# Kernel tuning notes

Measured on AMD Instinct MI355X. Metric: run time of the kernel, lower is better.

The kernel has to match this reference:

```python
import jax, jax.numpy as jnp
import numpy as np

N, E, B, DIM, NF, EF, HID = 16384, 32768, 512, 64, 14, 4, 128

def _p(key, shape, scale):
    return jax.random.normal(key, shape, dtype=jnp.float32) * scale

def setup_inputs() -> dict:
    key = jax.random.key(0)
    ks = jax.random.split(key, 20)
    s = lambda fan: 1.0 / float(np.sqrt(fan))
    z = lambda *sh: jnp.zeros(sh, jnp.float32)
    return {
        "x": jax.random.normal(ks[0], (N, NF), dtype=jnp.float32),
        "edge_index": jax.random.randint(ks[1], (2, E), 0, N),
        "edge_attr": jax.random.uniform(ks[2], (E, EF), dtype=jnp.float32),
        "batch": jnp.sort(jax.random.randint(ks[3], (N,), 0, B)),
        "do_dropout": 0,
        "mlp_drop": 0,
        "lin0_w": _p(ks[4], (NF, DIM), s(NF)), "lin0_b": z(DIM),
        "nn1_w": _p(ks[5], (EF, HID), s(EF)), "nn1_b": z(HID),
        "nn2_w": _p(ks[6], (HID, DIM * DIM), s(HID)), "nn2_b": z(DIM * DIM),
        "root_w": _p(ks[7], (DIM, DIM), s(DIM)), "conv_b": z(DIM),
        "gru_w_ih": _p(ks[8], (3 * DIM, DIM), s(DIM)), "gru_w_hh": _p(ks[9], (3 * DIM, DIM), s(DIM)),
        "gru_b_ih": _p(ks[10], (3 * DIM,), s(DIM)), "gru_b_hh": _p(ks[11], (3 * DIM,), s(DIM)),
        "lstm_w_ih": _p(ks[12], (4 * DIM, 2 * DIM), s(DIM)), "lstm_w_hh": _p(ks[13], (4 * DIM, DIM), s(DIM)),
        "lstm_b_ih": _p(ks[14], (4 * DIM,), s(DIM)), "lstm_b_hh": _p(ks[15], (4 * DIM,), s(DIM)),
        "lin1_w": _p(ks[16], (2 * DIM, DIM), s(2 * DIM)), "lin1_b": z(DIM),
        "lin2_w": _p(ks[17], (DIM, 1), s(DIM)), "lin2_b": z(1),
    }

def _forward(x, edge_attr, lin0_w, lin0_b, nn1_w, nn1_b, nn2_w, nn2_b, root_w, conv_b,
             gru_w_ih, gru_w_hh, gru_b_ih, gru_b_hh,
             lstm_w_ih, lstm_w_hh, lstm_b_ih, lstm_b_hh,
             lin1_w, lin1_b, lin2_w, lin2_b, edge_index, batch):
    src, dst = edge_index[0], edge_index[1]
    out = jax.nn.relu(x @ lin0_w + lin0_b)                      # [N, DIM]
    h = out
    # Edge-conditioned weights (edge_attr is layer-independent -> compute once)
    ew = jax.nn.relu(edge_attr @ nn1_w + nn1_b) @ nn2_w + nn2_b  # [E, DIM*DIM]
    ew = ew.reshape(E, DIM, DIM)
    deg = jax.ops.segment_sum(jnp.ones((E,), jnp.float32), dst, num_segments=N)
    deg = jnp.maximum(deg, 1.0)[:, None]                        # mean aggregation denominator

    def gru_cell(xin, hprev):
        gi = xin @ gru_w_ih.T + gru_b_ih
        gh = hprev @ gru_w_hh.T + gru_b_hh
        ir, iz, inn = jnp.split(gi, 3, axis=-1)
        hr, hz, hn = jnp.split(gh, 3, axis=-1)
        r = jax.nn.sigmoid(ir + hr)
        zg = jax.nn.sigmoid(iz + hz)
        n = jnp.tanh(inn + r * hn)
        return (1.0 - zg) * n + zg * hprev

    for _ in range(3):  # 3 message-passing rounds (structurally fixed)
        msg = jnp.einsum('ed,edf->ef', out[src], ew)            # gather -> per-edge matvec
        agg = jax.ops.segment_sum(msg, dst, num_segments=N) / deg
        m = jax.nn.relu(out @ root_w + agg + conv_b)            # NNConv (root weight + mean aggr)
        h = gru_cell(m, h)
        out = h

    # Set2Set pooling, 3 processing steps
    q_star = jnp.zeros((B, 2 * DIM), jnp.float32)
    hl = jnp.zeros((B, DIM), jnp.float32)
    cl = jnp.zeros((B, DIM), jnp.float32)
    for _ in range(3):
        gates = q_star @ lstm_w_ih.T + lstm_b_ih + hl @ lstm_w_hh.T + lstm_b_hh
        ii, ff, gg, oo = jnp.split(gates, 4, axis=-1)
        cl = jax.nn.sigmoid(ff) * cl + jax.nn.sigmoid(ii) * jnp.tanh(gg)
        hl = jax.nn.sigmoid(oo) * jnp.tanh(cl)
        q = hl                                                  # [B, DIM]
        e = jnp.sum(out * q[batch], axis=-1)                    # [N]
        emax = jax.ops.segment_max(e, batch, num_segments=B)
        ex = jnp.exp(e - emax[batch])
        esum = jnp.maximum(jax.ops.segment_sum(ex, batch, num_segments=B), 1e-16)
        a = ex / esum[batch]                                    # segment softmax
        r = jax.ops.segment_sum(a[:, None] * out, batch, num_segments=B)
        q_star = jnp.concatenate([q, r], axis=-1)               # [B, 2*DIM]

    y = jax.nn.relu(q_star @ lin1_w + lin1_b)
    # dropout flags are False (eval) -> identity
    y = y @ lin2_w + lin2_b
    return y.reshape(-1)                                        # [B]

def reference(x, edge_index, edge_attr, batch, do_dropout, mlp_drop,
              lin0_w, lin0_b, nn1_w, nn1_b, nn2_w, nn2_b, root_w, conv_b,
              gru_w_ih, gru_w_hh, gru_b_ih, gru_b_hh,
              lstm_w_ih, lstm_w_hh, lstm_b_ih, lstm_b_hh,
              lin1_w, lin1_b, lin2_w, lin2_b):
    return _forward(x, edge_attr, lin0_w, lin0_b, nn1_w, nn1_b, nn2_w, nn2_b, root_w, conv_b,
                    gru_w_ih, gru_w_hh, gru_b_ih, gru_b_hh,
                    lstm_w_ih, lstm_w_hh, lstm_b_ih, lstm_b_hh,
                    lin1_w, lin1_b, lin2_w, lin2_b, edge_index, batch)
```

## Files before the change

kernel.cpp:

```cpp
#include <hip/hip_runtime.h>
#include <math.h>

#define N_NODES 16384
#define N_EDGES 32768
#define NGRAPH  512
#define DIM     64
#define NF      14
#define HIDN    128
#define EWCOLS  4096

typedef unsigned short u16;
typedef unsigned int   u32;
typedef __attribute__((ext_vector_type(8))) short bf16x8;
typedef __attribute__((ext_vector_type(4))) float f32x4;
typedef __attribute__((ext_vector_type(4))) u32   u32x4;

__device__ inline float b2f(u16 u){
    unsigned int x = ((unsigned int)u) << 16;
    return __builtin_bit_cast(float, x);
}
__device__ inline u16 f2b(float f){
    unsigned int x = __builtin_bit_cast(unsigned int, f);
    unsigned int r = (x + 0x7FFFu + ((x >> 16) & 1u)) >> 16;
    return (u16)r;
}
__device__ inline float sigf(float x){ return 1.f / (1.f + expf(-x)); }

__global__ __launch_bounds__(256) void k_lin0(const float* __restrict__ x,
        const float* __restrict__ w, const float* __restrict__ b, float* __restrict__ out){
    int n = (blockIdx.x * blockDim.x + threadIdx.x) >> 6;
    int lane = threadIdx.x & 63;
    if (n >= N_NODES) return;
    float xv = (lane < NF) ? x[n * NF + lane] : 0.f;
    float acc = b[lane];
    #pragma unroll
    for (int d = 0; d < NF; ++d){
        float xd = __shfl(xv, d);
        acc += xd * w[d * DIM + lane];
    }
    out[n * DIM + lane] = fmaxf(acc, 0.f);
}

__global__ __launch_bounds__(256) void k_prep(const float* __restrict__ w2,
        const float* __restrict__ lwih, const float* __restrict__ lwhh,
        const float* __restrict__ root, const float* __restrict__ gwih, const float* __restrict__ gwhh,
        u16* __restrict__ w2T, float* __restrict__ wihT, float* __restrict__ whhT,
        u16* __restrict__ rtHi, u16* __restrict__ rtLo,
        u16* __restrict__ wihHi, u16* __restrict__ wihLo,
        u16* __restrict__ whhHi, u16* __restrict__ whhLo){
    int i = blockIdx.x * 256 + threadIdx.x;
    if (i < 524288){
        int k = i >> 12, c = i & 4095;
        w2T[c * HIDN + k] = f2b(w2[i]);
    } else if (i < 557056){
        int i2 = i - 524288;
        int j = i2 >> 7, d = i2 & 127;
        wihT[d * 256 + j] = lwih[i2];
    } else if (i < 573440){
        int i2 = i - 557056;
        int j = i2 >> 6, d = i2 & 63;
        whhT[d * 256 + j] = lwhh[i2];
    } else if (i < 577536){
        int i2 = i - 573440;
        int d = i2 >> 6, j = i2 & 63;
        float v = root[i2]; u16 h = f2b(v);
        rtHi[j * 64 + d] = h; rtLo[j * 64 + d] = f2b(v - b2f(h));
    } else if (i < 589824){
        int k = i - 577536;
        float v = gwih[k]; u16 h = f2b(v);
        wihHi[k] = h; wihLo[k] = f2b(v - b2f(h));
    } else if (i < 602112){
        int k = i - 589824;
        float v = gwhh[k]; u16 h = f2b(v);
        whhHi[k] = h; whhLo[k] = f2b(v - b2f(h));
    }
}

__global__ __launch_bounds__(256) void k_deg(const int* __restrict__ ei, unsigned* __restrict__ degu){
    int e = blockIdx.x * blockDim.x + threadIdx.x;
    if (e < N_EDGES) atomicAdd(&degu[ei[N_EDGES + e]], 1u);
}
__global__ __launch_bounds__(256) void k_dinv(const unsigned* __restrict__ degu, float* __restrict__ dinv){
    int n = blockIdx.x * blockDim.x + threadIdx.x;
    if (n < N_NODES) dinv[n] = 1.f / fmaxf((float)degu[n], 1.f);
}

#define EB   128
#define LDO  68

__global__ __launch_bounds__(512) void k_msg_fused(
        const int* __restrict__ ei, const float* __restrict__ ea,
        const float* __restrict__ w1, const float* __restrict__ b1,
        const u16* __restrict__ w2T, const float* __restrict__ b2,
        const float* __restrict__ out, float* __restrict__ agg)
{
    __shared__ float s_out[EB * LDO];
    __shared__ u16   s_b[2][64 * 128];
    __shared__ float s_b2[EWCOLS];
    __shared__ float s_w1[512];
    __shared__ float s_b1[128];
    int tid = threadIdx.x;
    int e0 = blockIdx.x * EB;

    s_w1[tid] = w1[tid];
    if (tid < 128) s_b1[tid] = b1[tid];
    {
        int base = tid * 8;
        *(float4*)(s_b2 + base)     = *(const float4*)(b2 + base);
        *(float4*)(s_b2 + base + 4) = *(const float4*)(b2 + base + 4);
    }
    {
        int row = tid >> 2, cb = (tid & 3) * 16;
        int s = ei[e0 + row];
        const float4* sp = (const float4*)(out + (size_t)s * DIM + cb);
        float4 v0 = sp[0], v1 = sp[1], v2 = sp[2], v3 = sp[3];
        float* dst = s_out + row * LDO + cb;
        *(float4*)(dst)      = v0;
        *(float4*)(dst + 4)  = v1;
        *(float4*)(dst + 8)  = v2;
        *(float4*)(dst + 12) = v3;
    }
    __syncthreads();

    int wv = tid >> 6, lane = tid & 63;
    int WR = (wv >> 1) * 32, WC = (wv & 1) * 32;
    int lr = lane & 15, lk = (lane >> 4) * 8;

    bf16x8 afr[2][4];
    #pragma unroll
    for (int m = 0; m < 2; ++m){
        int erow = e0 + WR + m*16 + lr;
        float4 av = *(const float4*)(ea + (size_t)erow * 4);
        #pragma unroll
        for (int kk = 0; kk < 4; ++kk){
            bf16x8 t8;
            #pragma unroll
            for (int i = 0; i < 8; ++i){
                int h = kk*32 + lk + i;
                float acc = s_b1[h] + av.x*s_w1[h] + av.y*s_w1[128+h]
                          + av.z*s_w1[256+h] + av.w*s_w1[384+h];
                t8[i] = (short)f2b(fmaxf(acc, 0.f));
            }
            afr[m][kk] = t8;
        }
    }

    int bc = tid >> 3, bs = tid & 7;
    const u32x4* gb = (const u32x4*)w2T;
    u32x4 r0 = gb[((size_t)bc << 4) + bs*2];
    u32x4 r1 = gb[((size_t)bc << 4) + bs*2 + 1];

    f32x4 msg[2][2] = {};
    int swzr = (lr & 7) << 4;
    int swzw = (bc & 7) << 4;
    int crow = (lane >> 4) * 4;

    for (int d = 0; d < 64; ++d){
        char* sw = (char*)s_b[d & 1];
        *(u32x4*)(sw + ((bc*256 + bs*32)      ^ swzw)) = r0;
        *(u32x4*)(sw + ((bc*256 + bs*32 + 16) ^ swzw)) = r1;
        if (d < 63){
            size_t base = ((size_t)(d+1)*64 + bc) << 4;
            r0 = gb[base + bs*2];
            r1 = gb[base + bs*2 + 1];
        }
        __syncthreads();
        const char* sr = (const char*)s_b[d & 1];
        f32x4 ew[2][2] = {};
        #pragma unroll
        for (int kk = 0; kk < 4; ++kk){
            int kb = kk*64 + (lane >> 4) * 16;
            bf16x8 bf0 = *(const bf16x8*)(sr + (((WC + lr)*256 + kb)      ^ swzr));
            bf16x8 bf1 = *(const bf16x8*)(sr + (((WC + 16 + lr)*256 + kb) ^ swzr));
            ew[0][0] = __builtin_amdgcn_mfma_f32_16x16x32_bf16(afr[0][kk], bf0, ew[0][0], 0, 0, 0);
            ew[0][1] = __builtin_amdgcn_mfma_f32_16x16x32_bf16(afr[0][kk], bf1, ew[0][1], 0, 0, 0);
            ew[1][0] = __builtin_amdgcn_mfma_f32_16x16x32_bf16(afr[1][kk], bf0, ew[1][0], 0, 0, 0);
            ew[1][1] = __builtin_amdgcn_mfma_f32_16x16x32_bf16(afr[1][kk], bf1, ew[1][1], 0, 0, 0);
        }
        float b2v0 = s_b2[d*64 + WC + lr];
        float b2v1 = s_b2[d*64 + WC + 16 + lr];
        #pragma unroll
        for (int m = 0; m < 2; ++m){
            #pragma unroll
            for (int r = 0; r < 4; ++r){
                float sc = s_out[(WR + m*16 + crow + r) * LDO + d];
                msg[m][0][r] += sc * (ew[m][0][r] + b2v0);
                msg[m][1][r] += sc * (ew[m][1][r] + b2v1);
            }
        }
    }

    #pragma unroll
    for (int m = 0; m < 2; ++m){
        #pragma unroll
        for (int r = 0; r < 4; ++r){
            int eg = e0 + WR + m*16 + crow + r;
            int dn = ei[N_EDGES + eg];
            atomicAdd(&agg[(size_t)dn * DIM + WC + lr],      msg[m][0][r]);
            atomicAdd(&agg[(size_t)dn * DIM + WC + 16 + lr], msg[m][1][r]);
        }
    }
}

#define LDH 68
__global__ __launch_bounds__(256) void k_update(
        const u16* __restrict__ rtHi, const u16* __restrict__ rtLo,
        const u16* __restrict__ wihHi, const u16* __restrict__ wihLo,
        const u16* __restrict__ whhHi, const u16* __restrict__ whhLo,
        const float* __restrict__ convb, const float* __restrict__ bih,
        const float* __restrict__ bhh,
        const float* __restrict__ agg, const float* __restrict__ dinv,
        float* __restrict__ out)
{
    __shared__ float s_h[64 * LDH];
    __shared__ float s_aux[64 * LDH];
    __shared__ float s_m[64 * LDH];
    int tid = threadIdx.x;
    int n0 = blockIdx.x * 64;

    {
        int row = tid >> 2, cb = (tid & 3) * 16;
        const float4* hp = (const float4*)(out + (size_t)(n0 + row) * DIM + cb);
        const float4* ap = (const float4*)(agg + (size_t)(n0 + row) * DIM + cb);
        float di = dinv[n0 + row];
        #pragma unroll
        for (int q = 0; q < 4; ++q){
            float4 hv = hp[q];
            float4 av = ap[q];
            *(float4*)(s_h + row * LDH + cb + q*4) = hv;
            float4 xv;
            xv.x = av.x * di + convb[cb + q*4 + 0];
            xv.y = av.y * di + convb[cb + q*4 + 1];
            xv.z = av.z * di + convb[cb + q*4 + 2];
            xv.w = av.w * di + convb[cb + q*4 + 3];
            *(float4*)(s_aux + row * LDH + cb + q*4) = xv;
        }
    }
    __syncthreads();

    int wv = tid >> 6, lane = tid & 63;
    int lr = lane & 15, lkb = (lane >> 4) * 8;
    int arow = wv * 16 + lr;

    bf16x8 hHi[2], hLo[2];
    #pragma unroll
    for (int kk = 0; kk < 2; ++kk){
        const float* src = s_h + arow * LDH + kk*32 + lkb;
        bf16x8 hi8, lo8;
        #pragma unroll
        for (int e = 0; e < 8; ++e){
            float v = src[e];
            u16 h = f2b(v);
            hi8[e] = (short)h;
            lo8[e] = (short)f2b(v - b2f(h));
        }
        hHi[kk] = hi8; hLo[kk] = lo8;
    }

    f32x4 c1[4] = {};
    #pragma unroll
    for (int ct = 0; ct < 4; ++ct){
        #pragma unroll
        for (int kk = 0; kk < 2; ++kk){
            int off = (ct*16 + lr) * 64 + kk*32 + lkb;
            bf16x8 bHi = *(const bf16x8*)(rtHi + off);
            bf16x8 bLo = *(const bf16x8*)(rtLo + off);
            c1[ct] = __builtin_amdgcn_mfma_f32_16x16x32_bf16(hHi[kk], bHi, c1[ct], 0, 0, 0);
            c1[ct] = __builtin_amdgcn_mfma_f32_16x16x32_bf16(hLo[kk], bHi, c1[ct], 0, 0, 0);
            c1[ct] = __builtin_amdgcn_mfma_f32_16x16x32_bf16(hHi[kk], bLo, c1[ct], 0, 0, 0);
        }
    }

    int crow = (lane >> 4) * 4;
    #pragma unroll
    for (int ct = 0; ct < 4; ++ct){
        #pragma unroll
        for (int r = 0; r < 4; ++r){
            int row = wv*16 + crow + r;
            int col = ct*16 + lr;
            float m = fmaxf(c1[ct][r] + s_aux[row * LDH + col], 0.f);
            s_m[row * LDH + col] = m;
        }
    }
    __syncthreads();

    bf16x8 mHi[2], mLo[2];
    #pragma unroll
    for (int kk = 0; kk < 2; ++kk){
        const float* src = s_m + arow * LDH + kk*32 + lkb;
        bf16x8 hi8, lo8;
        #pragma unroll
        for (int e = 0; e < 8; ++e){
            float v = src[e];
            u16 h = f2b(v);
            hi8[e] = (short)h;
            lo8[e] = (short)f2b(v - b2f(h));
        }
        mHi[kk] = hi8; mLo[kk] = lo8;
    }

    f32x4 gi[12] = {}, gh[12] = {};
    #pragma unroll
    for (int ct = 0; ct < 12; ++ct){
        #pragma unroll
        for (int kk = 0; kk < 2; ++kk){
            int off = (ct*16 + lr) * 64 + kk*32 + lkb;
            bf16x8 biH = *(const bf16x8*)(wihHi + off);
            bf16x8 biL = *(const bf16x8*)(wihLo + off);
            gi[ct] = __builtin_amdgcn_mfma_f32_16x16x32_bf16(mHi[kk], biH, gi[ct], 0, 0, 0);
            gi[ct] = __builtin_amdgcn_mfma_f32_16x16x32_bf16(mLo[kk], biH, gi[ct], 0, 0, 0);
            gi[ct] = __builtin_amdgcn_mfma_f32_16x16x32_bf16(mHi[kk], biL, gi[ct], 0, 0, 0);
            bf16x8 bhH = *(const bf16x8*)(whhHi + off);
            bf16x8 bhL = *(const bf16x8*)(whhLo + off);
            gh[ct] = __builtin_amdgcn_mfma_f32_16x16x32_bf16(hHi[kk], bhH, gh[ct], 0, 0, 0);
            gh[ct] = __builtin_amdgcn_mfma_f32_16x16x32_bf16(hLo[kk], bhH, gh[ct], 0, 0, 0);
            gh[ct] = __builtin_amdgcn_mfma_f32_16x16x32_bf16(hHi[kk], bhL, gh[ct], 0, 0, 0);
        }
    }

    #pragma unroll
    for (int ct = 0; ct < 4; ++ct){
        int col = ct*16 + lr;
        float br_i = bih[col],       br_h = bhh[col];
        float bz_i = bih[64 + col],  bz_h = bhh[64 + col];
        float bn_i = bih[128 + col], bn_h = bhh[128 + col];
        #pragma unroll
        for (int r = 0; r < 4; ++r){
            int row = wv*16 + crow + r;
            float rg = sigf(gi[ct][r] + br_i + gh[ct][r] + br_h);
            float zg = sigf(gi[ct+4][r] + bz_i + gh[ct+4][r] + bz_h);
            float ng = tanhf(gi[ct+8][r] + bn_i + rg * (gh[ct+8][r] + bn_h));
            float h  = s_h[row * LDH + col];
            s_aux[row * LDH + col] = (1.f - zg) * ng + zg * h;
        }
    }
    __syncthreads();

    {
        int row = tid >> 2, cb = (tid & 3) * 16;
        #pragma unroll
        for (int q = 0; q < 4; ++q)
            *(float4*)(out + (size_t)(n0 + row) * DIM + cb + q*4) =
                *(const float4*)(s_aux + row * LDH + cb + q*4);
    }
}

__global__ __launch_bounds__(256) void k_s2s(
        const float* __restrict__ out, const int* __restrict__ batch,
        const float* __restrict__ wihT, const float* __restrict__ lbih,
        const float* __restrict__ whhT, const float* __restrict__ lbhh,
        const float* __restrict__ l1w, const float* __restrict__ l1b,
        const float* __restrict__ l2w, const float* __restrict__ l2b,
        float* __restrict__ y)
{
    __shared__ float s_q[128];
    __shared__ float s_hc[128];
    __shared__ float s_g[256];
    __shared__ float s_rw[256];
    __shared__ float s_sw[8];
    __shared__ int   s_rng[2];
    int g = blockIdx.x, tid = threadIdx.x;
    if (tid < 2){
        int target = g + tid;
        int lo = 0, hi = N_NODES;
        while (lo < hi){ int mid = (lo + hi) >> 1; if (batch[mid] < target) lo = mid + 1; else hi = mid; }
        s_rng[tid] = lo;
    }
    if (tid < 128){ s_q[tid] = 0.f; s_hc[tid] = 0.f; }
    __syncthreads();
    int s0 = s_rng[0], s1 = s_rng[1];
    int wv = tid >> 6, lane = tid & 63;

    for (int step = 0; step < 3; ++step){
        float acc = lbih[tid] + lbhh[tid];
        #pragma unroll 8
        for (int d = 0; d < 128; ++d) acc += s_q[d] * wihT[d * 256 + tid];
        #pragma unroll 8
        for (int d = 0; d < 64;  ++d) acc += s_hc[d] * whhT[d * 256 + tid];
        s_g[tid] = acc;
        __syncthreads();
        if (tid < 64){
            float c = sigf(s_g[64 + tid]) * s_hc[64 + tid] + sigf(s_g[tid]) * tanhf(s_g[128 + tid]);
            float h = sigf(s_g[192 + tid]) * tanhf(c);
            s_hc[tid] = h; s_hc[64 + tid] = c;
            s_q[tid] = h;
        }
        __syncthreads();
        float q = s_hc[lane];
        float emx = -3.4e38f;
        for (int n = s0 + wv; n < s1; n += 4){
            float v = out[(size_t)n * DIM + lane] * q;
            #pragma unroll
            for (int off = 32; off; off >>= 1) v += __shfl_xor(v, off);
            emx = fmaxf(emx, v);
        }
        if (lane == 0) s_sw[wv] = emx;
        __syncthreads();
        float gmax = fmaxf(fmaxf(s_sw[0], s_sw[1]), fmaxf(s_sw[2], s_sw[3]));
        float rl = 0.f, ss = 0.f;
        for (int n = s0 + wv; n < s1; n += 4){
            float o = out[(size_t)n * DIM + lane];
            float v = o * q;
            #pragma unroll
            for (int off = 32; off; off >>= 1) v += __shfl_xor(v, off);
            float ex = expf(v - gmax);
            rl += ex * o;
            ss += ex;
        }
        s_rw[wv * 64 + lane] = rl;
        if (lane == 0) s_sw[4 + wv] = ss;
        __syncthreads();
        if (tid < 64){
            float r = s_rw[tid] + s_rw[64 + tid] + s_rw[128 + tid] + s_rw[192 + tid];
            float S = fmaxf(s_sw[4] + s_sw[5] + s_sw[6] + s_sw[7], 1e-16f);
            s_q[64 + tid] = r / S;
        }
        __syncthreads();
    }
    if (wv == 0){
        float acc = l1b[lane];
        #pragma unroll 8
        for (int d = 0; d < 128; ++d) acc += s_q[d] * l1w[d * 64 + lane];
        float h = fmaxf(acc, 0.f);
        float p = h * l2w[lane];
        #pragma unroll
        for (int off = 32; off; off >>= 1) p += __shfl_down(p, off);
        if (lane == 0) y[g] = p + l2b[0];
    }
}

extern "C" void kernel_launch(void* const* d_in, const int* in_sizes, int n_in,
                              void* d_out, int out_size, void* d_ws, size_t ws_size,
                              hipStream_t stream){
    const float* x      = (const float*)d_in[0];
    const int*   ei     = (const int*)d_in[1];
    const float* ea     = (const float*)d_in[2];
    const int*   batch  = (const int*)d_in[3];
    const float* lin0_w = (const float*)d_in[6];
    const float* lin0_b = (const float*)d_in[7];
    const float* nn1_w  = (const float*)d_in[8];
    const float* nn1_b  = (const float*)d_in[9];
    const float* nn2_w  = (const float*)d_in[10];
    const float* nn2_b  = (const float*)d_in[11];
    const float* root_w = (const float*)d_in[12];
    const float* conv_b = (const float*)d_in[13];
    const float* gwih   = (const float*)d_in[14];
    const float* gwhh   = (const float*)d_in[15];
    const float* gbih   = (const float*)d_in[16];
    const float* gbhh   = (const float*)d_in[17];
    const float* lwih   = (const float*)d_in[18];
    const float* lwhh   = (const float*)d_in[19];
    const float* lbih   = (const float*)d_in[20];
    const float* lbhh   = (const float*)d_in[21];
    const float* l1w    = (const float*)d_in[22];
    const float* l1b    = (const float*)d_in[23];
    const float* l2w    = (const float*)d_in[24];
    const float* l2b    = (const float*)d_in[25];
    float* y = (float*)d_out;

    char* p = (char*)d_ws;
    float* out   = (float*)p;    p += (size_t)N_NODES * DIM * 4;
    float* agg   = (float*)p;    p += (size_t)N_NODES * DIM * 4;
    u16* w2T     = (u16*)p;      p += (size_t)EWCOLS * HIDN * 2;
    float* wihT  = (float*)p;    p += 128 * 256 * 4;
    float* whhT  = (float*)p;    p += 64 * 256 * 4;
    u16* rtHi    = (u16*)p;      p += 4096 * 2;
    u16* rtLo    = (u16*)p;      p += 4096 * 2;
    u16* wihHi   = (u16*)p;      p += 12288 * 2;
    u16* wihLo   = (u16*)p;      p += 12288 * 2;
    u16* whhHi   = (u16*)p;      p += 12288 * 2;
    u16* whhLo   = (u16*)p;      p += 12288 * 2;
    unsigned* degu = (unsigned*)p; p += N_NODES * 4;
    float* dinv  = (float*)p;    p += N_NODES * 4;

    if ((size_t)(p - (char*)d_ws) > ws_size) return;

    hipMemsetAsync(degu, 0, N_NODES * 4, stream);

    k_prep<<<2352, 256, 0, stream>>>(nn2_w, lwih, lwhh, root_w, gwih, gwhh,
                w2T, wihT, whhT, rtHi, rtLo, wihHi, wihLo, whhHi, whhLo);
    k_lin0<<<N_NODES / 4, 256, 0, stream>>>(x, lin0_w, lin0_b, out);
    k_deg <<<N_EDGES / 256, 256, 0, stream>>>(ei, degu);
    k_dinv<<<N_NODES / 256, 256, 0, stream>>>(degu, dinv);

    for (int r = 0; r < 3; ++r){
        hipMemsetAsync(agg, 0, (size_t)N_NODES * DIM * 4, stream);
        k_msg_fused<<<N_EDGES / EB, 512, 0, stream>>>(ei, ea, nn1_w, nn1_b, w2T, nn2_b, out, agg);
        k_update   <<<N_NODES / 64, 256, 0, stream>>>(rtHi, rtLo, wihHi, wihLo, whhHi, whhLo,
                        conv_b, gbih, gbhh, agg, dinv, out);
    }

    k_s2s<<<NGRAPH, 256, 0, stream>>>(out, batch, wihT, lbih, whhT, lbhh,
                l1w, l1b, l2w, l2b, y);
}
```

Measured before the change: 300.9 us.

## Load MFMA B fragments directly from global memory, removing LDS staging and barriers

The message kernel no longer stages the bf16 nn2 weight slices through double-buffered shared memory with a block barrier every iteration. Each wave now reads its MFMA B fragments straight from global memory (expected to be L2-resident) into registers, using software double buffering across pairs of d iterations. This removes 64 __syncthreads and 16 KB of LDS per block, which may raise occupancy. In exchange, each wave issues redundant global loads for the same weight data and register pressure rises.

```diff
diff --git a/kernel.cpp b/kernel.cpp
--- a/kernel.cpp
+++ b/kernel.cpp
@@ -95,7 +95,6 @@
         const float* __restrict__ out, float* __restrict__ agg)
 {
     __shared__ float s_out[EB * LDO];
-    __shared__ u16   s_b[2][64 * 128];
     __shared__ float s_b2[EWCOLS];
     __shared__ float s_w1[512];
     __shared__ float s_b1[128];
@@ -125,6 +124,7 @@
     int wv = tid >> 6, lane = tid & 63;
     int WR = (wv >> 1) * 32, WC = (wv & 1) * 32;
     int lr = lane & 15, lk = (lane >> 4) * 8;
+    int l16 = lane >> 4;
 
     bf16x8 afr[2][4];
     #pragma unroll
@@ -145,50 +145,54 @@
         }
     }
 
-    int bc = tid >> 3, bs = tid & 7;
     const u32x4* gb = (const u32x4*)w2T;
-    u32x4 r0 = gb[((size_t)bc << 4) + bs*2];
-    u32x4 r1 = gb[((size_t)bc << 4) + bs*2 + 1];
-
+    int rowA = WC + lr;
+    int rowB = WC + 16 + lr;
+    int crow = (lane >> 4) * 4;
     f32x4 msg[2][2] = {};
-    int swzr = (lr & 7) << 4;
-    int swzw = (bc & 7) << 4;
-    int crow = (lane >> 4) * 4;
-
-    for (int d = 0; d < 64; ++d){
-        char* sw = (char*)s_b[d & 1];
-        *(u32x4*)(sw + ((bc*256 + bs*32)      ^ swzw)) = r0;
-        *(u32x4*)(sw + ((bc*256 + bs*32 + 16) ^ swzw)) = r1;
-        if (d < 63){
-            size_t base = ((size_t)(d+1)*64 + bc) << 4;
-            r0 = gb[base + bs*2];
-            r1 = gb[base + bs*2 + 1];
-        }
-        __syncthreads();
-        const char* sr = (const char*)s_b[d & 1];
-        f32x4 ew[2][2] = {};
-        #pragma unroll
-        for (int kk = 0; kk < 4; ++kk){
-            int kb = kk*64 + (lane >> 4) * 16;
-            bf16x8 bf0 = *(const bf16x8*)(sr + (((WC + lr)*256 + kb)      ^ swzr));
-            bf16x8 bf1 = *(const bf16x8*)(sr + (((WC + 16 + lr)*256 + kb) ^ swzr));
-            ew[0][0] = __builtin_amdgcn_mfma_f32_16x16x32_bf16(afr[0][kk], bf0, ew[0][0], 0, 0, 0);
-            ew[0][1] = __builtin_amdgcn_mfma_f32_16x16x32_bf16(afr[0][kk], bf1, ew[0][1], 0, 0, 0);
-            ew[1][0] = __builtin_amdgcn_mfma_f32_16x16x32_bf16(afr[1][kk], bf0, ew[1][0], 0, 0, 0);
-            ew[1][1] = __builtin_amdgcn_mfma_f32_16x16x32_bf16(afr[1][kk], bf1, ew[1][1], 0, 0, 0);
-        }
-        float b2v0 = s_b2[d*64 + WC + lr];
-        float b2v1 = s_b2[d*64 + WC + 16 + lr];
-        #pragma unroll
-        for (int m = 0; m < 2; ++m){
-            #pragma unroll
-            for (int r = 0; r < 4; ++r){
-                float sc = s_out[(WR + m*16 + crow + r) * LDO + d];
-                msg[m][0][r] += sc * (ew[m][0][r] + b2v0);
-                msg[m][1][r] += sc * (ew[m][1][r] + b2v1);
-            }
-        }
-    }
+
+    u32x4 fA[2][4], fB[2][4];
+
+#define LOADF(F, dd) { \
+    int b0 = (((dd)*64 + rowA) << 4) + l16; \
+    int b1i = (((dd)*64 + rowB) << 4) + l16; \
+    F[0][0] = gb[b0];      F[0][1] = gb[b0 + 4]; \
+    F[0][2] = gb[b0 + 8];  F[0][3] = gb[b0 + 12]; \
+    F[1][0] = gb[b1i];     F[1][1] = gb[b1i + 4]; \
+    F[1][2] = gb[b1i + 8]; F[1][3] = gb[b1i + 12]; }
+
+#define COMPUTE(F, dd) { \
+    f32x4 ew00 = {}, ew01 = {}, ew10 = {}, ew11 = {}; \
+    _Pragma("unroll") \
+    for (int kk = 0; kk < 4; ++kk){ \
+        bf16x8 bf0 = __builtin_bit_cast(bf16x8, F[0][kk]); \
+        bf16x8 bf1 = __builtin_bit_cast(bf16x8, F[1][kk]); \
+        ew00 = __builtin_amdgcn_mfma_f32_16x16x32_bf16(afr[0][kk], bf0, ew00, 0, 0, 0); \
+        ew01 = __builtin_amdgcn_mfma_f32_16x16x32_bf16(afr[0][kk], bf1, ew01, 0, 0, 0); \
+        ew10 = __builtin_amdgcn_mfma_f32_16x16x32_bf16(afr[1][kk], bf0, ew10, 0, 0, 0); \
+        ew11 = __builtin_amdgcn_mfma_f32_16x16x32_bf16(afr[1][kk], bf1, ew11, 0, 0, 0); \
+    } \
+    float b2v0 = s_b2[(dd)*64 + WC + lr]; \
+    float b2v1 = s_b2[(dd)*64 + WC + 16 + lr]; \
+    _Pragma("unroll") \
+    for (int r = 0; r < 4; ++r){ \
+        float sc0 = s_out[(WR + crow + r) * LDO + (dd)]; \
+        float sc1 = s_out[(WR + 16 + crow + r) * LDO + (dd)]; \
+        msg[0][0][r] += sc0 * (ew00[r] + b2v0); \
+        msg[0][1][r] += sc0 * (ew01[r] + b2v1); \
+        msg[1][0][r] += sc1 * (ew10[r] + b2v0); \
+        msg[1][1][r] += sc1 * (ew11[r] + b2v1); \
+    } }
+
+    LOADF(fA, 0);
+    for (int d = 0; d < 64; d += 2){
+        LOADF(fB, d + 1);
+        COMPUTE(fA, d);
+        if (d + 2 < 64) LOADF(fA, d + 2);
+        COMPUTE(fB, d + 1);
+    }
+#undef LOADF
+#undef COMPUTE
 
     #pragma unroll
     for (int m = 0; m < 2; ++m){
```

Result: slower. 519.5 us (+72.6%).

## Pipeline W2 staging with one barrier per step, hoist bias term, fold agg zeroing

Applied to the files above, without the earlier changes.

Restructures the message kernel's inner loop: the next W2 slice is written to the alternate LDS buffer before computing the current one, with a manual waitcnt plus raw s_barrier, and the global prefetch is issued two steps ahead. The nn2 bias contribution is pulled out of the 64-step loop into a separate epilogue that reads b2 straight from global memory, which frees 16KB of LDS and removes per-step bias adds. The per-layer memset of agg is replaced by k_update zeroing agg after reading it, leaving a single initial memset. The hand-written barrier and waitcnt sequence is a correctness risk, and the bias epilogue adds extra global reads.

```diff
diff --git a/kernel.cpp b/kernel.cpp
--- a/kernel.cpp
+++ b/kernel.cpp
@@ -96,19 +96,18 @@
 {
     __shared__ float s_out[EB * LDO];
     __shared__ u16   s_b[2][64 * 128];
-    __shared__ float s_b2[EWCOLS];
     __shared__ float s_w1[512];
     __shared__ float s_b1[128];
     int tid = threadIdx.x;
     int e0 = blockIdx.x * EB;
 
+    int bc = tid >> 3, bs = tid & 7;
+    const u32x4* gb = (const u32x4*)w2T;
+    u32x4 r0 = gb[((size_t)bc << 4) + bs*2];
+    u32x4 r1 = gb[((size_t)bc << 4) + bs*2 + 1];
+
     s_w1[tid] = w1[tid];
     if (tid < 128) s_b1[tid] = b1[tid];
-    {
-        int base = tid * 8;
-        *(float4*)(s_b2 + base)     = *(const float4*)(b2 + base);
-        *(float4*)(s_b2 + base + 4) = *(const float4*)(b2 + base + 4);
-    }
     {
         int row = tid >> 2, cb = (tid & 3) * 16;
         int s = ei[e0 + row];
@@ -145,48 +144,76 @@
         }
     }
 
-    int bc = tid >> 3, bs = tid & 7;
-    const u32x4* gb = (const u32x4*)w2T;
-    u32x4 r0 = gb[((size_t)bc << 4) + bs*2];
-    u32x4 r1 = gb[((size_t)bc << 4) + bs*2 + 1];
-
-    f32x4 msg[2][2] = {};
+    int swzw = (bc & 7) << 4;
     int swzr = (lr & 7) << 4;
-    int swzw = (bc & 7) << 4;
     int crow = (lane >> 4) * 4;
 
-    for (int d = 0; d < 64; ++d){
-        char* sw = (char*)s_b[d & 1];
+    {
+        char* sw = (char*)s_b[0];
         *(u32x4*)(sw + ((bc*256 + bs*32)      ^ swzw)) = r0;
         *(u32x4*)(sw + ((bc*256 + bs*32 + 16) ^ swzw)) = r1;
+        size_t base = ((size_t)64 + bc) << 4;
+        r0 = gb[base + bs*2];
+        r1 = gb[base + bs*2 + 1];
+    }
+    asm volatile("s_waitcnt lgkmcnt(0)" ::: "memory");
+    __builtin_amdgcn_sched_barrier(0);
+    __builtin_amdgcn_s_barrier();
+    __builtin_amdgcn_sched_barrier(0);
+
+    f32x4 msg[2][2] = {};
+
+    for (int d = 0; d < 64; ++d){
         if (d < 63){
-            size_t base = ((size_t)(d+1)*64 + bc) << 4;
-            r0 = gb[base + bs*2];
-            r1 = gb[base + bs*2 + 1];
-        }
-        __syncthreads();
+            char* sw = (char*)s_b[(d + 1) & 1];
+            *(u32x4*)(sw + ((bc*256 + bs*32)      ^ swzw)) = r0;
+            *(u32x4*)(sw + ((bc*256 + bs*32 + 16) ^ swzw)) = r1;
+            if (d < 62){
+                size_t base = ((size_t)(d + 2) * 64 + bc) << 4;
+                r0 = gb[base + bs*2];
+                r1 = gb[base + bs*2 + 1];
+            }
+        }
         const char* sr = (const char*)s_b[d & 1];
-        f32x4 ew[2][2] = {};
+        f32x4 ew00 = {}, ew01 = {}, ew10 = {}, ew11 = {};
         #pragma unroll
         for (int kk = 0; kk < 4; ++kk){
             int kb = kk*64 + (lane >> 4) * 16;
             bf16x8 bf0 = *(const bf16x8*)(sr + (((WC + lr)*256 + kb)      ^ swzr));
             bf16x8 bf1 = *(const bf16x8*)(sr + (((WC + 16 + lr)*256 + kb) ^ swzr));
-            ew[0][0] = __builtin_amdgcn_mfma_f32_16x16x32_bf16(afr[0][kk], bf0, ew[0][0], 0, 0, 0);
-            ew[0][1] = __builtin_amdgcn_mfma_f32_16x16x32_bf16(afr[0][kk], bf1, ew[0][1], 0, 0, 0);
-            ew[1][0] = __builtin_amdgcn_mfma_f32_16x16x32_bf16(afr[1][kk], bf0, ew[1][0], 0, 0, 0);
-            ew[1][1] = __builtin_amdgcn_mfma_f32_16x16x32_bf16(afr[1][kk], bf1, ew[1][1], 0, 0, 0);
-        }
-        float b2v0 = s_b2[d*64 + WC + lr];
-        float b2v1 = s_b2[d*64 + WC + 16 + lr];
-        #pragma unroll
-        for (int m = 0; m < 2; ++m){
-            #pragma unroll
-            for (int r = 0; r < 4; ++r){
-                float sc = s_out[(WR + m*16 + crow + r) * LDO + d];
-                msg[m][0][r] += sc * (ew[m][0][r] + b2v0);
-                msg[m][1][r] += sc * (ew[m][1][r] + b2v1);
-            }
+            ew00 = __builtin_amdgcn_mfma_f32_16x16x32_bf16(afr[0][kk], bf0, ew00, 0, 0, 0);
+            ew01 = __builtin_amdgcn_mfma_f32_16x16x32_bf16(afr[0][kk], bf1, ew01, 0, 0, 0);
+            ew10 = __builtin_amdgcn_mfma_f32_16x16x32_bf16(afr[1][kk], bf0, ew10, 0, 0, 0);
+            ew11 = __builtin_amdgcn_mfma_f32_16x16x32_bf16(afr[1][kk], bf1, ew11, 0, 0, 0);
+        }
+        #pragma unroll
+        for (int r = 0; r < 4; ++r){
+            float sc0 = s_out[(WR + crow + r) * LDO + d];
+            float sc1 = s_out[(WR + 16 + crow + r) * LDO + d];
+            msg[0][0][r] += sc0 * ew00[r];
+            msg[0][1][r] += sc0 * ew01[r];
+            msg[1][0][r] += sc1 * ew10[r];
+            msg[1][1][r] += sc1 * ew11[r];
+        }
+        asm volatile("s_waitcnt lgkmcnt(0)" ::: "memory");
+        __builtin_amdgcn_sched_barrier(0);
+        __builtin_amdgcn_s_barrier();
+        __builtin_amdgcn_sched_barrier(0);
+    }
+
+    int f0 = WC + lr;
+    #pragma unroll 8
+    for (int dd = 0; dd < 64; ++dd){
+        float bv0 = b2[dd*64 + f0];
+        float bv1 = b2[dd*64 + f0 + 16];
+        #pragma unroll
+        for (int r = 0; r < 4; ++r){
+            float sc0 = s_out[(WR + crow + r) * LDO + dd];
+            float sc1 = s_out[(WR + 16 + crow + r) * LDO + dd];
+            msg[0][0][r] += sc0 * bv0;
+            msg[0][1][r] += sc0 * bv1;
+            msg[1][0][r] += sc1 * bv0;
+            msg[1][1][r] += sc1 * bv1;
         }
     }
 
@@ -209,7 +236,7 @@
         const u16* __restrict__ whhHi, const u16* __restrict__ whhLo,
         const float* __restrict__ convb, const float* __restrict__ bih,
         const float* __restrict__ bhh,
-        const float* __restrict__ agg, const float* __restrict__ dinv,
+        float* __restrict__ agg, const float* __restrict__ dinv,
         float* __restrict__ out)
 {
     __shared__ float s_h[64 * LDH];
@@ -221,12 +248,14 @@
     {
         int row = tid >> 2, cb = (tid & 3) * 16;
         const float4* hp = (const float4*)(out + (size_t)(n0 + row) * DIM + cb);
-        const float4* ap = (const float4*)(agg + (size_t)(n0 + row) * DIM + cb);
+        float4* ap = (float4*)(agg + (size_t)(n0 + row) * DIM + cb);
         float di = dinv[n0 + row];
+        float4 zv = {0.f, 0.f, 0.f, 0.f};
         #pragma unroll
         for (int q = 0; q < 4; ++q){
             float4 hv = hp[q];
             float4 av = ap[q];
+            ap[q] = zv;
             *(float4*)(s_h + row * LDH + cb + q*4) = hv;
             float4 xv;
             xv.x = av.x * di + convb[cb + q*4 + 0];
@@ -476,6 +505,7 @@
     if ((size_t)(p - (char*)d_ws) > ws_size) return;
 
     hipMemsetAsync(degu, 0, N_NODES * 4, stream);
+    hipMemsetAsync(agg, 0, (size_t)N_NODES * DIM * 4, stream);
 
     k_prep<<<2352, 256, 0, stream>>>(nn2_w, lwih, lwhh, root_w, gwih, gwhh,
                 w2T, wihT, whhT, rtHi, rtLo, wihHi, wihLo, whhHi, whhLo);
@@ -484,7 +514,6 @@
     k_dinv<<<N_NODES / 256, 256, 0, stream>>>(degu, dinv);
 
     for (int r = 0; r < 3; ++r){
-        hipMemsetAsync(agg, 0, (size_t)N_NODES * DIM * 4, stream);
         k_msg_fused<<<N_EDGES / EB, 512, 0, stream>>>(ei, ea, nn1_w, nn1_b, w2T, nn2_b, out, agg);
         k_update   <<<N_NODES / 64, 256, 0, stream>>>(rtHi, rtLo, wihHi, wihLo, whhHi, whhLo,
                         conv_b, gbih, gbhh, agg, dinv, out);
```

Result: slower. 321.7 us (+6.9%).

## Split K across waves in fused message kernel to halve B-fragment LDS reads

Applied to the files above, without the earlier changes.

Reorganizes the 8 waves of the fused edge-message kernel so each wave covers 64 edge rows by 32 columns over half of the hidden K dimension (split-K), instead of 32x32 over the full K. Each wave now reuses each B fragment across four M tiles, which cuts LDS reads per MFMA. The partial sums from the two K halves are combined through the existing atomicAdd into agg, with the bias applied only by the kg==0 half. This doubles the atomic traffic and the per-wave message accumulators, so register pressure rises. The launch bounds now also request 2 blocks per CU.

```diff
diff --git a/kernel.cpp b/kernel.cpp
--- a/kernel.cpp
+++ b/kernel.cpp
@@ -88,7 +88,7 @@
 #define EB   128
 #define LDO  68
 
-__global__ __launch_bounds__(512) void k_msg_fused(
+__global__ __launch_bounds__(512, 2) void k_msg_fused(
         const int* __restrict__ ei, const float* __restrict__ ea,
         const float* __restrict__ w1, const float* __restrict__ b1,
         const u16* __restrict__ w2T, const float* __restrict__ b2,
@@ -123,20 +123,27 @@
     __syncthreads();
 
     int wv = tid >> 6, lane = tid & 63;
-    int WR = (wv >> 1) * 32, WC = (wv & 1) * 32;
-    int lr = lane & 15, lk = (lane >> 4) * 8;
-
-    bf16x8 afr[2][4];
-    #pragma unroll
-    for (int m = 0; m < 2; ++m){
+    int kg = wv & 1;
+    int cg = (wv >> 1) & 1;
+    int rg = wv >> 2;
+    int WR = rg * 64;
+    int WC = cg * 32;
+    int KB = kg * 64;
+    int lr = lane & 15;
+    int hi = lane >> 4;
+    int lk = hi * 8;
+
+    bf16x8 afr[4][2];
+    #pragma unroll
+    for (int m = 0; m < 4; ++m){
         int erow = e0 + WR + m*16 + lr;
         float4 av = *(const float4*)(ea + (size_t)erow * 4);
         #pragma unroll
-        for (int kk = 0; kk < 4; ++kk){
+        for (int kk = 0; kk < 2; ++kk){
             bf16x8 t8;
             #pragma unroll
             for (int i = 0; i < 8; ++i){
-                int h = kk*32 + lk + i;
+                int h = KB + kk*32 + lk + i;
                 float acc = s_b1[h] + av.x*s_w1[h] + av.y*s_w1[128+h]
                           + av.z*s_w1[256+h] + av.w*s_w1[384+h];
                 t8[i] = (short)f2b(fmaxf(acc, 0.f));
@@ -150,10 +157,11 @@
     u32x4 r0 = gb[((size_t)bc << 4) + bs*2];
     u32x4 r1 = gb[((size_t)bc << 4) + bs*2 + 1];
 
-    f32x4 msg[2][2] = {};
+    f32x4 msg[4][2] = {};
     int swzr = (lr & 7) << 4;
     int swzw = (bc & 7) << 4;
-    int crow = (lane >> 4) * 4;
+    int crow = hi * 4;
+    float kgf = (kg == 0) ? 1.f : 0.f;
 
     for (int d = 0; d < 64; ++d){
         char* sw = (char*)s_b[d & 1];
@@ -166,21 +174,22 @@
         }
         __syncthreads();
         const char* sr = (const char*)s_b[d & 1];
-        f32x4 ew[2][2] = {};
-        #pragma unroll
-        for (int kk = 0; kk < 4; ++kk){
-            int kb = kk*64 + (lane >> 4) * 16;
+        f32x4 ew[4][2] = {};
+        #pragma unroll
+        for (int kk = 0; kk < 2; ++kk){
+            int kb = KB*2 + kk*64 + hi*16;
             bf16x8 bf0 = *(const bf16x8*)(sr + (((WC + lr)*256 + kb)      ^ swzr));
             bf16x8 bf1 = *(const bf16x8*)(sr + (((WC + 16 + lr)*256 + kb) ^ swzr));
-            ew[0][0] = __builtin_amdgcn_mfma_f32_16x16x32_bf16(afr[0][kk], bf0, ew[0][0], 0, 0, 0);
-            ew[0][1] = __builtin_amdgcn_mfma_f32_16x16x32_bf16(afr[0][kk], bf1, ew[0][1], 0, 0, 0);
-            ew[1][0] = __builtin_amdgcn_mfma_f32_16x16x32_bf16(afr[1][kk], bf0, ew[1][0], 0, 0, 0);
-            ew[1][1] = __builtin_amdgcn_mfma_f32_16x16x32_bf16(afr[1][kk], bf1, ew[1][1], 0, 0, 0);
-        }
-        float b2v0 = s_b2[d*64 + WC + lr];
-        float b2v1 = s_b2[d*64 + WC + 16 + lr];
-        #pragma unroll
-        for (int m = 0; m < 2; ++m){
+            #pragma unroll
+            for (int m = 0; m < 4; ++m){
+                ew[m][0] = __builtin_amdgcn_mfma_f32_16x16x32_bf16(afr[m][kk], bf0, ew[m][0], 0, 0, 0);
+                ew[m][1] = __builtin_amdgcn_mfma_f32_16x16x32_bf16(afr[m][kk], bf1, ew[m][1], 0, 0, 0);
+            }
+        }
+        float b2v0 = s_b2[d*64 + WC + lr] * kgf;
+        float b2v1 = s_b2[d*64 + WC + 16 + lr] * kgf;
+        #pragma unroll
+        for (int m = 0; m < 4; ++m){
             #pragma unroll
             for (int r = 0; r < 4; ++r){
                 float sc = s_out[(WR + m*16 + crow + r) * LDO + d];
@@ -191,7 +200,7 @@
     }
 
     #pragma unroll
-    for (int m = 0; m < 2; ++m){
+    for (int m = 0; m < 4; ++m){
         #pragma unroll
         for (int r = 0; r < 4; ++r){
             int eg = e0 + WR + m*16 + crow + r;
```

Result: slower. 326.5 us (+8.5%).
